# Performance work log

Measured on AMD Instinct MI355X. Metric: run time of the kernel, lower is better.

## Reference

```python
import jax, jax.numpy as jnp
import numpy as np

N_NODES = 50000
N_EDGES = 800000
DIM = 64
N_LAYERS = 5


def setup_inputs() -> dict:
    key = jax.random.key(0)
    k1, k2, k3, k4, k5 = jax.random.split(key, 5)
    x = jax.random.normal(k1, (N_NODES, DIM), dtype=jnp.float32)
    # 3 weight matrices per GIN layer (2 hidden + 1 output Dense, all [dim,dim], relu, no bias)
    W = jax.random.normal(k2, (N_LAYERS, 3, DIM, DIM), dtype=jnp.float32) * (1.0 / np.sqrt(DIM))
    # per-layer read-out Dense(1, use_bias=False)
    Wl = jax.random.normal(k3, (N_LAYERS, DIM), dtype=jnp.float32) * (1.0 / np.sqrt(DIM))
    src = jax.random.randint(k4, (N_EDGES,), 0, N_NODES, dtype=jnp.int32)
    dst = jax.random.randint(k5, (N_EDGES,), 0, N_NODES, dtype=jnp.int32)
    return {"x": x, "W": W, "Wl": Wl, "src": src, "dst": dst}


def reference(x, W, Wl, src, dst):
    n = x.shape[0]
    h = x
    pooled = []  # per-layer global mean pool  [dim]
    for i in range(N_LAYERS):
        agg = h + jax.ops.segment_sum(h[src], dst, num_segments=n)  # (1+eps)*h + sum_neighbors
        h = jax.nn.relu(agg @ W[i, 0])
        h = jax.nn.relu(h @ W[i, 1])
        h = jax.nn.relu(h @ W[i, 2])
        pooled.append(jnp.mean(h, axis=0))
    # stack per-layer Dense(1) read-outs, sum over layers, sigmoid -> shape [1]
    logits = jnp.einsum("ld,ld->l", jnp.stack(pooled), Wl)  # [5]
    return jax.nn.sigmoid(jnp.sum(logits)[None])
```

## Files before the change

kernel.cpp:

```cpp
#include <hip/hip_runtime.h>
#include <hip/hip_fp16.h>
#include <math.h>

#define N_NODES 50000
#define N_EDGES 800000
#define DIM 64
#define N_LAYERS 5

#define BLK 128
#define ROWS 32
#define HSTRIDE 68
#define POOL_REP 16

#define NB 196
#define CAPB 5632
#define EPB (N_EDGES / 256)

#define EBCAP 512

#define WFRAG_PER_LAYER (3 * 2 * 4 * 64 * 8)
#define XP (N_NODES * DIM / 4)
#define WP (N_LAYERS * WFRAG_PER_LAYER)

typedef __attribute__((ext_vector_type(8))) short short8;
typedef __attribute__((ext_vector_type(4))) float floatx4;

__device__ inline unsigned short bf16_rne(float f) {
    unsigned int u = __float_as_uint(f);
    return (unsigned short)((u + 0x7FFFu + ((u >> 16) & 1u)) >> 16);
}
__device__ inline float bf16_f(unsigned short h) {
    return __uint_as_float(((unsigned int)h) << 16);
}
__device__ inline float e5m2_f32(unsigned char b) {
    return __half2float(__ushort_as_half((unsigned short)((unsigned short)b << 8)));
}
__device__ inline unsigned char f32_e5m2(float f) {
    unsigned short us = __half_as_ushort(__float2half(f));
    us = (unsigned short)(us + 0x7F + ((us >> 8) & 1));
    return (unsigned char)(us >> 8);
}
__device__ inline __half2 e5m2x2_lo(unsigned d) {
    unsigned h = __builtin_amdgcn_perm(0u, d, 0x01050004u);
    return __builtin_bit_cast(__half2, h);
}
__device__ inline __half2 e5m2x2_hi(unsigned d) {
    unsigned h = __builtin_amdgcn_perm(0u, d, 0x03070206u);
    return __builtin_bit_cast(__half2, h);
}

__global__ __launch_bounds__(256) void prep_kernel(const float* __restrict__ x,
                                                   const float* __restrict__ W,
                                                   unsigned char* __restrict__ x8,
                                                   unsigned short* __restrict__ wfrag,
                                                   int* __restrict__ bucketCnt,
                                                   float* __restrict__ pooled) {
    int i = blockIdx.x * 256 + threadIdx.x;
    if (i < XP) {
        float4 v = ((const float4*)x)[i];
        uchar4 u;
        u.x = f32_e5m2(v.x); u.y = f32_e5m2(v.y);
        u.z = f32_e5m2(v.z); u.w = f32_e5m2(v.w);
        ((uchar4*)x8)[i] = u;
        return;
    }
    i -= XP;
    if (i < WP) {
        int t = i;
        int j    = t & 7;
        int lane = (t >> 3) & 63;
        int nt   = (t >> 9) & 3;
        int kt   = (t >> 11) & 1;
        int rest = t >> 12;
        int p    = rest % 3;
        int layer= rest / 3;
        int k = kt * 32 + (lane >> 4) * 8 + j;
        int n = nt * 16 + (lane & 15);
        float v = W[(((size_t)layer * 3 + p) * 64 + k) * 64 + n];
        wfrag[t] = bf16_rne(v);
        return;
    }
    i -= WP;
    if (i < NB) { bucketCnt[i] = 0; return; }
    i -= NB;
    if (i < N_LAYERS * POOL_REP * DIM) pooled[i] = 0.f;
}

__global__ __launch_bounds__(256) void bfill2_kernel(const int* __restrict__ src,
                                                     const int* __restrict__ dst,
                                                     int* __restrict__ bucketCnt,
                                                     int* __restrict__ ebuf) {
    __shared__ int cnt[NB];
    __shared__ int basev[NB];
    const int t = threadIdx.x;
    const int e0 = blockIdx.x * EPB;
    if (t < NB) cnt[t] = 0;
    __syncthreads();
    for (int i = t; i < EPB; i += 256)
        atomicAdd(&cnt[dst[e0 + i] >> 8], 1);
    __syncthreads();
    if (t < NB) {
        int c = cnt[t];
        basev[t] = c ? atomicAdd(&bucketCnt[t], c) : 0;
        cnt[t] = 0;
    }
    __syncthreads();
    for (int i = t; i < EPB; i += 256) {
        int d = dst[e0 + i];
        int b = d >> 8;
        int pos = atomicAdd(&cnt[b], 1);
        ebuf[(size_t)b * CAPB + basev[b] + pos] = ((d & 255) << 16) | src[e0 + i];
    }
}

__global__ __launch_bounds__(256) void bbuild_kernel(const int* __restrict__ ebuf,
                                                     const int* __restrict__ bucketCnt,
                                                     int* __restrict__ rowptr,
                                                     int* __restrict__ csr_src) {
    __shared__ int red[256];
    __shared__ int cnt[256];
    __shared__ int scan[256];
    __shared__ int cur[256];
    __shared__ int lds_e[CAPB];
    const int t = threadIdx.x;
    const int b = blockIdx.x;

    red[t] = (t < b && t < NB) ? bucketCnt[t] : 0;
    __syncthreads();
    #pragma unroll
    for (int off = 128; off > 0; off >>= 1) {
        if (t < off) red[t] += red[t + off];
        __syncthreads();
    }
    const int base  = red[0];
    const int cnt_b = bucketCnt[b];
    const int* __restrict__ ereg = ebuf + (size_t)b * CAPB;

    cnt[t] = 0;
    __syncthreads();
    for (int i = t; i < cnt_b; i += 256) {
        int v = ereg[i];
        lds_e[i] = v;
        atomicAdd(&cnt[v >> 16], 1);
    }
    __syncthreads();
    scan[t] = cnt[t];
    __syncthreads();
    #pragma unroll
    for (int off = 1; off < 256; off <<= 1) {
        int u = (t >= off) ? scan[t - off] : 0;
        __syncthreads();
        scan[t] += u;
        __syncthreads();
    }
    int excl = scan[t] - cnt[t];
    rowptr[b * 256 + t] = base + excl;
    cur[t] = excl;
    __syncthreads();
    for (int i = t; i < cnt_b; i += 256) {
        int v = lds_e[i];
        int pos = atomicAdd(&cur[v >> 16], 1);
        csr_src[base + pos] = v & 0xFFFF;
    }
}

__global__ __launch_bounds__(BLK) void layer_kernel(const unsigned char* __restrict__ h8,
                                                    const int* __restrict__ rowptr,
                                                    const int* __restrict__ csr_src,
                                                    const unsigned short* __restrict__ wf,
                                                    unsigned char* __restrict__ h_out,
                                                    float* __restrict__ pooled) {
    __shared__ float H[ROWS * HSTRIDE];
    __shared__ int EB[2][EBCAP];
    const int tid  = threadIdx.x;
    const int lane = tid & 63;
    const int w    = __builtin_amdgcn_readfirstlane(tid >> 6);
    const int n0   = blockIdx.x * ROWS;
    const int nw   = n0 + w * 16;
    const int c4   = (lane & 15) << 2;
    const int q    = lane >> 4;

    int rpv = rowptr[nw + min(lane, 16)];
    const int e0w  = __builtin_amdgcn_readlane(rpv, 0);
    const int span = __builtin_amdgcn_readlane(rpv, 16) - e0w;

    if (span <= EBCAP) {
        for (int i = lane; i < span; i += 64)
            EB[w][i] = csr_src[e0w + i];
        asm volatile("s_waitcnt lgkmcnt(0)" ::: "memory");
        const int* eb = &EB[w][0];

        for (int g = 0; g < 4; ++g) {
            const int myrow = 4 * g + q;
            const int e0q = __shfl(rpv, myrow, 64);
            const int deg = __shfl(rpv, myrow + 1, 64) - e0q;
            int Rm = deg;
            Rm = max(Rm, __shfl_xor(Rm, 16, 64));
            Rm = max(Rm, __shfl_xor(Rm, 32, 64));
            const int Rpad = (Rm + 7) & ~7;
            const int rowq = nw + myrow;
            const int ob   = e0q - e0w;

            __half2 a01 = __float2half2_rn(0.f);
            __half2 a23 = __float2half2_rn(0.f);

            for (int i = 0; i < Rpad; i += 8) {
                unsigned dv[8];
                #pragma unroll
                for (int k = 0; k < 8; ++k) {
                    int ev = eb[ob + i + k];
                    int s  = (i + k < deg) ? ev : rowq;
                    dv[k] = *(const unsigned*)(h8 + (((unsigned)s << 6) | (unsigned)c4));
                }
                #pragma unroll
                for (int k = 0; k < 8; ++k) {
                    a01 = __hadd2(a01, e5m2x2_lo(dv[k]));
                    a23 = __hadd2(a23, e5m2x2_hi(dv[k]));
                }
            }

            unsigned sd = *(const unsigned*)(h8 + (((unsigned)rowq << 6) | (unsigned)c4));
            float scale = (float)(1 - (Rpad - deg));
            float2 f01 = __half22float2(a01);
            float2 f23 = __half22float2(a23);
            float4 r;
            r.x = f01.x + e5m2_f32((unsigned char)(sd      )) * scale;
            r.y = f01.y + e5m2_f32((unsigned char)(sd >>  8)) * scale;
            r.z = f23.x + e5m2_f32((unsigned char)(sd >> 16)) * scale;
            r.w = f23.y + e5m2_f32((unsigned char)(sd >> 24)) * scale;
            if (rowq >= N_NODES) { r.x = 0.f; r.y = 0.f; r.z = 0.f; r.w = 0.f; }
            *(float4*)&H[(w * 16 + myrow) * HSTRIDE + c4] = r;
        }
    } else {
        for (int j = 0; j < 16; ++j) {
            const int n = nw + j;
            const int e0 = __builtin_amdgcn_readlane(rpv, j);
            const int e1 = __builtin_amdgcn_readlane(rpv, j + 1);
            float acc = 0.f;
            if (n < N_NODES) {
                float self = e5m2_f32(h8[(size_t)n * DIM + lane]);
                acc = self;
                for (int base = e0; base < e1; base += 64) {
                    const int m  = min(64, e1 - base);
                    const int mr = (m + 3) & ~3;
                    int idx = (lane < m) ? csr_src[base + lane] : n;
                    acc -= (float)(mr - m) * self;
                    for (int jj = 0; jj < mr; jj += 4) {
                        int s0 = __builtin_amdgcn_readlane(idx, jj + 0);
                        int s1 = __builtin_amdgcn_readlane(idx, jj + 1);
                        int s2 = __builtin_amdgcn_readlane(idx, jj + 2);
                        int s3 = __builtin_amdgcn_readlane(idx, jj + 3);
                        float v0 = e5m2_f32(h8[(size_t)s0 * DIM + lane]);
                        float v1 = e5m2_f32(h8[(size_t)s1 * DIM + lane]);
                        float v2 = e5m2_f32(h8[(size_t)s2 * DIM + lane]);
                        float v3 = e5m2_f32(h8[(size_t)s3 * DIM + lane]);
                        acc += (v0 + v1) + (v2 + v3);
                    }
                }
            }
            H[(w * 16 + j) * HSTRIDE + lane] = acc;
        }
    }
    __syncthreads();

    const int mrow = lane & 15;
    const int quad = lane >> 4;
    const short8* Bf = (const short8*)wf;

    for (int p = 0; p < 3; ++p) {
        short8 Ahi[2];
        #pragma unroll
        for (int kt = 0; kt < 2; ++kt) {
            const float* ap = &H[(w * 16 + mrow) * HSTRIDE + kt * 32 + quad * 8];
            float4 f0 = *(const float4*)ap;
            float4 f1 = *(const float4*)(ap + 4);
            float fv[8] = {f0.x, f0.y, f0.z, f0.w, f1.x, f1.y, f1.z, f1.w};
            short8 hi;
            #pragma unroll
            for (int jj = 0; jj < 8; ++jj)
                hi[jj] = (short)bf16_rne(fv[jj]);
            Ahi[kt] = hi;
        }

        floatx4 acc[4];
        #pragma unroll
        for (int nt = 0; nt < 4; ++nt) { acc[nt][0]=0.f; acc[nt][1]=0.f; acc[nt][2]=0.f; acc[nt][3]=0.f; }

        #pragma unroll
        for (int nt = 0; nt < 4; ++nt) {
            #pragma unroll
            for (int kt = 0; kt < 2; ++kt) {
                int fbase = ((p * 2 + kt) * 4 + nt) * 64 + lane;
                short8 bhi = Bf[fbase];
                acc[nt] = __builtin_amdgcn_mfma_f32_16x16x32_bf16(Ahi[kt], bhi, acc[nt], 0, 0, 0);
            }
        }
        __syncthreads();
        #pragma unroll
        for (int nt = 0; nt < 4; ++nt) {
            #pragma unroll
            for (int reg = 0; reg < 4; ++reg) {
                int row = w * 16 + quad * 4 + reg;
                H[row * HSTRIDE + nt * 16 + mrow] = fmaxf(acc[nt][reg], 0.f);
            }
        }
        __syncthreads();
    }

    #pragma unroll
    for (int i = 0; i < 4; ++i) {
        int t4 = tid + i * BLK;
        int r  = t4 >> 4;
        int c  = (t4 & 15) << 2;
        int grow = n0 + r;
        if (grow < N_NODES) {
            float4 v = *(const float4*)&H[r * HSTRIDE + c];
            uchar4 u;
            u.x = f32_e5m2(v.x); u.y = f32_e5m2(v.y);
            u.z = f32_e5m2(v.z); u.w = f32_e5m2(v.w);
            *(uchar4*)(h_out + (size_t)grow * DIM + c) = u;
        }
    }

    if (tid < 64) {
        float s = 0.f;
        #pragma unroll
        for (int r = 0; r < ROWS; ++r)
            s += H[r * HSTRIDE + tid];
        atomicAdd(&pooled[(blockIdx.x & (POOL_REP - 1)) * DIM + tid], s);
    }
}

__global__ void finalize_kernel(const float* __restrict__ pooled,
                                const float* __restrict__ Wl,
                                float* __restrict__ out) {
    int c = threadIdx.x;
    float s = 0.f;
    #pragma unroll
    for (int l = 0; l < N_LAYERS; ++l) {
        float col = 0.f;
        #pragma unroll
        for (int r = 0; r < POOL_REP; ++r)
            col += pooled[(l * POOL_REP + r) * DIM + c];
        s += col * Wl[l * DIM + c];
    }
    #pragma unroll
    for (int off = 32; off > 0; off >>= 1)
        s += __shfl_down(s, off, 64);
    if (c == 0) {
        float logit = s / (float)N_NODES;
        out[0] = 1.f / (1.f + expf(-logit));
    }
}

extern "C" void kernel_launch(void* const* d_in, const int* in_sizes, int n_in,
                              void* d_out, int out_size, void* d_ws, size_t ws_size,
                              hipStream_t stream) {
    const float* x   = (const float*)d_in[0];
    const float* W   = (const float*)d_in[1];
    const float* Wl  = (const float*)d_in[2];
    const int*   src = (const int*)d_in[3];
    const int*   dst = (const int*)d_in[4];
    float* out = (float*)d_out;

    char* ws = (char*)d_ws;
    const size_t h8Bytes = (size_t)N_NODES * DIM;
    unsigned char* hX = (unsigned char*)(ws);
    unsigned char* hA = (unsigned char*)(ws + h8Bytes);
    unsigned char* hB = (unsigned char*)(ws + 2 * h8Bytes);
    int*   csr_src  = (int*)  (ws + 3 * h8Bytes);
    int*   ebuf     = csr_src + N_EDGES;
    int*   rowptr   = ebuf + (size_t)NB * CAPB;
    int*   bucketCnt= rowptr + NB * 256;
    float* pooled   = (float*)(bucketCnt + NB);
    unsigned short* wfrag = (unsigned short*)(pooled + N_LAYERS * POOL_REP * DIM);

    const int prepItems = XP + WP + NB + N_LAYERS * POOL_REP * DIM;
    prep_kernel<<<(prepItems + 255) / 256, 256, 0, stream>>>(x, W, hX, wfrag, bucketCnt, pooled);
    bfill2_kernel<<<256, 256, 0, stream>>>(src, dst, bucketCnt, ebuf);
    bbuild_kernel<<<NB, 256, 0, stream>>>(ebuf, bucketCnt, rowptr, csr_src);

    const unsigned char* hcur = hX;
    unsigned char* hnext = hA;
    const int grid = (N_NODES + ROWS - 1) / ROWS;
    for (int l = 0; l < N_LAYERS; ++l) {
        layer_kernel<<<grid, BLK, 0, stream>>>(
            hcur, rowptr, csr_src, wfrag + (size_t)l * WFRAG_PER_LAYER, hnext,
            pooled + (size_t)l * POOL_REP * DIM);
        hcur = hnext;
        hnext = (hnext == hA) ? hB : hA;
    }
    finalize_kernel<<<1, 64, 0, stream>>>(pooled, Wl, out);
}
```

Measured before the change: 192.8 us.

## Widen gather loads, pre-shift CSR indices, drop block barriers, retune CSR build

The gather phase now has each lane load 8 bytes (uint2) covering 8 features, so each group of 8 lanes serves one row and a wave walks 16 rows in two passes instead of four. Source indices are stored pre-shifted by 6 in LDS to save address arithmetic. The per-MLP-layer __syncthreads are replaced by wave-local LDS waits, relying on each wave only touching its own 16 rows. The CSR build now uses 512 fill blocks and a 512-thread build kernel with shuffle-based reductions and scans instead of LDS tree loops. Together these aim to cut gather instruction count, barrier stalls and preprocessing latency, at some risk of LDS ordering hazards if any cross-wave sharing remains.

Result: faster. 186.4 us (-3.3%).

```diff
diff --git a/kernel.cpp b/kernel.cpp
--- a/kernel.cpp
+++ b/kernel.cpp
@@ -14,7 +14,8 @@
 
 #define NB 196
 #define CAPB 5632
-#define EPB (N_EDGES / 256)
+#define BF2_BLOCKS 512
+#define EPB2 ((N_EDGES + BF2_BLOCKS - 1) / BF2_BLOCKS)
 
 #define EBCAP 512
 
@@ -28,9 +29,6 @@
 __device__ inline unsigned short bf16_rne(float f) {
     unsigned int u = __float_as_uint(f);
     return (unsigned short)((u + 0x7FFFu + ((u >> 16) & 1u)) >> 16);
-}
-__device__ inline float bf16_f(unsigned short h) {
-    return __uint_as_float(((unsigned int)h) << 16);
 }
 __device__ inline float e5m2_f32(unsigned char b) {
     return __half2float(__ushort_as_half((unsigned short)((unsigned short)b << 8)));
@@ -93,11 +91,13 @@
     __shared__ int cnt[NB];
     __shared__ int basev[NB];
     const int t = threadIdx.x;
-    const int e0 = blockIdx.x * EPB;
+    const int e0 = blockIdx.x * EPB2;
     if (t < NB) cnt[t] = 0;
     __syncthreads();
-    for (int i = t; i < EPB; i += 256)
-        atomicAdd(&cnt[dst[e0 + i] >> 8], 1);
+    for (int i = t; i < EPB2; i += 256) {
+        int e = e0 + i;
+        if (e < N_EDGES) atomicAdd(&cnt[dst[e] >> 8], 1);
+    }
     __syncthreads();
     if (t < NB) {
         int c = cnt[t];
@@ -105,62 +105,73 @@
         cnt[t] = 0;
     }
     __syncthreads();
-    for (int i = t; i < EPB; i += 256) {
-        int d = dst[e0 + i];
-        int b = d >> 8;
-        int pos = atomicAdd(&cnt[b], 1);
-        ebuf[(size_t)b * CAPB + basev[b] + pos] = ((d & 255) << 16) | src[e0 + i];
-    }
-}
-
-__global__ __launch_bounds__(256) void bbuild_kernel(const int* __restrict__ ebuf,
+    for (int i = t; i < EPB2; i += 256) {
+        int e = e0 + i;
+        if (e < N_EDGES) {
+            int d = dst[e];
+            int b = d >> 8;
+            int pos = atomicAdd(&cnt[b], 1);
+            ebuf[(size_t)b * CAPB + basev[b] + pos] = ((d & 255) << 16) | src[e];
+        }
+    }
+}
+
+__global__ __launch_bounds__(512) void bbuild_kernel(const int* __restrict__ ebuf,
                                                      const int* __restrict__ bucketCnt,
                                                      int* __restrict__ rowptr,
                                                      int* __restrict__ csr_src) {
-    __shared__ int red[256];
     __shared__ int cnt[256];
-    __shared__ int scan[256];
     __shared__ int cur[256];
+    __shared__ int wred[8];
+    __shared__ int wscan[4];
     __shared__ int lds_e[CAPB];
     const int t = threadIdx.x;
+    const int lane = t & 63;
+    const int wv = t >> 6;
     const int b = blockIdx.x;
 
-    red[t] = (t < b && t < NB) ? bucketCnt[t] : 0;
-    __syncthreads();
+    int v = (t < b && t < NB) ? bucketCnt[t] : 0;
     #pragma unroll
-    for (int off = 128; off > 0; off >>= 1) {
-        if (t < off) red[t] += red[t + off];
-        __syncthreads();
-    }
-    const int base  = red[0];
+    for (int off = 32; off > 0; off >>= 1) v += __shfl_xor(v, off, 64);
+    if (lane == 0) wred[wv] = v;
+    if (t < 256) cnt[t] = 0;
+    __syncthreads();
+    const int base  = wred[0] + wred[1] + wred[2] + wred[3];
     const int cnt_b = bucketCnt[b];
     const int* __restrict__ ereg = ebuf + (size_t)b * CAPB;
 
-    cnt[t] = 0;
-    __syncthreads();
-    for (int i = t; i < cnt_b; i += 256) {
-        int v = ereg[i];
-        lds_e[i] = v;
-        atomicAdd(&cnt[v >> 16], 1);
-    }
-    __syncthreads();
-    scan[t] = cnt[t];
-    __syncthreads();
-    #pragma unroll
-    for (int off = 1; off < 256; off <<= 1) {
-        int u = (t >= off) ? scan[t - off] : 0;
-        __syncthreads();
-        scan[t] += u;
-        __syncthreads();
-    }
-    int excl = scan[t] - cnt[t];
-    rowptr[b * 256 + t] = base + excl;
-    cur[t] = excl;
-    __syncthreads();
-    for (int i = t; i < cnt_b; i += 256) {
-        int v = lds_e[i];
-        int pos = atomicAdd(&cur[v >> 16], 1);
-        csr_src[base + pos] = v & 0xFFFF;
+    for (int i = t; i < cnt_b; i += 512) {
+        int e = ereg[i];
+        lds_e[i] = e;
+        atomicAdd(&cnt[e >> 16], 1);
+    }
+    __syncthreads();
+
+    int excl = 0;
+    if (t < 256) {
+        int s = cnt[t];
+        #pragma unroll
+        for (int off = 1; off < 64; off <<= 1) {
+            int u = __shfl_up(s, off, 64);
+            if (lane >= off) s += u;
+        }
+        if (lane == 63) wscan[wv] = s;
+        excl = s - cnt[t];
+    }
+    __syncthreads();
+    if (t < 256) {
+        int woff = 0;
+        #pragma unroll
+        for (int j = 0; j < 4; ++j) if (j < wv) woff += wscan[j];
+        excl += woff;
+        rowptr[b * 256 + t] = base + excl;
+        cur[t] = excl;
+    }
+    __syncthreads();
+    for (int i = t; i < cnt_b; i += 512) {
+        int e = lds_e[i];
+        int pos = atomicAdd(&cur[e >> 16], 1);
+        csr_src[base + pos] = e & 0xFFFF;
     }
 }
 
@@ -177,8 +188,8 @@
     const int w    = __builtin_amdgcn_readfirstlane(tid >> 6);
     const int n0   = blockIdx.x * ROWS;
     const int nw   = n0 + w * 16;
-    const int c4   = (lane & 15) << 2;
-    const int q    = lane >> 4;
+    const int o8   = (lane & 7) << 3;
+    const int rg   = lane >> 3;
 
     int rpv = rowptr[nw + min(lane, 16)];
     const int e0w  = __builtin_amdgcn_readlane(rpv, 0);
@@ -186,50 +197,63 @@
 
     if (span <= EBCAP) {
         for (int i = lane; i < span; i += 64)
-            EB[w][i] = csr_src[e0w + i];
+            EB[w][i] = csr_src[e0w + i] << 6;
         asm volatile("s_waitcnt lgkmcnt(0)" ::: "memory");
         const int* eb = &EB[w][0];
 
-        for (int g = 0; g < 4; ++g) {
-            const int myrow = 4 * g + q;
+        for (int g = 0; g < 2; ++g) {
+            const int myrow = g * 8 + rg;
             const int e0q = __shfl(rpv, myrow, 64);
             const int deg = __shfl(rpv, myrow + 1, 64) - e0q;
             int Rm = deg;
+            Rm = max(Rm, __shfl_xor(Rm, 8, 64));
             Rm = max(Rm, __shfl_xor(Rm, 16, 64));
             Rm = max(Rm, __shfl_xor(Rm, 32, 64));
             const int Rpad = (Rm + 7) & ~7;
             const int rowq = nw + myrow;
+            const int rq6  = rowq << 6;
             const int ob   = e0q - e0w;
 
             __half2 a01 = __float2half2_rn(0.f);
-            __half2 a23 = __float2half2_rn(0.f);
+            __half2 a23 = a01, a45 = a01, a67 = a01;
 
             for (int i = 0; i < Rpad; i += 8) {
-                unsigned dv[8];
+                uint2 dv[8];
                 #pragma unroll
                 for (int k = 0; k < 8; ++k) {
-                    int ev = eb[ob + i + k];
-                    int s  = (i + k < deg) ? ev : rowq;
-                    dv[k] = *(const unsigned*)(h8 + (((unsigned)s << 6) | (unsigned)c4));
+                    int s6 = eb[ob + i + k];
+                    s6 = (i + k < deg) ? s6 : rq6;
+                    dv[k] = *(const uint2*)(h8 + (unsigned)(s6 | o8));
                 }
                 #pragma unroll
                 for (int k = 0; k < 8; ++k) {
-                    a01 = __hadd2(a01, e5m2x2_lo(dv[k]));
-                    a23 = __hadd2(a23, e5m2x2_hi(dv[k]));
+                    a01 = __hadd2(a01, e5m2x2_lo(dv[k].x));
+                    a23 = __hadd2(a23, e5m2x2_hi(dv[k].x));
+                    a45 = __hadd2(a45, e5m2x2_lo(dv[k].y));
+                    a67 = __hadd2(a67, e5m2x2_hi(dv[k].y));
                 }
             }
 
-            unsigned sd = *(const unsigned*)(h8 + (((unsigned)rowq << 6) | (unsigned)c4));
+            uint2 sd = *(const uint2*)(h8 + (unsigned)(rq6 | o8));
             float scale = (float)(1 - (Rpad - deg));
-            float2 f01 = __half22float2(a01);
-            float2 f23 = __half22float2(a23);
-            float4 r;
-            r.x = f01.x + e5m2_f32((unsigned char)(sd      )) * scale;
-            r.y = f01.y + e5m2_f32((unsigned char)(sd >>  8)) * scale;
-            r.z = f23.x + e5m2_f32((unsigned char)(sd >> 16)) * scale;
-            r.w = f23.y + e5m2_f32((unsigned char)(sd >> 24)) * scale;
-            if (rowq >= N_NODES) { r.x = 0.f; r.y = 0.f; r.z = 0.f; r.w = 0.f; }
-            *(float4*)&H[(w * 16 + myrow) * HSTRIDE + c4] = r;
+            float2 f01 = __half22float2(a01), f23 = __half22float2(a23);
+            float2 f45 = __half22float2(a45), f67 = __half22float2(a67);
+            float4 r0, r1;
+            r0.x = f01.x + e5m2_f32((unsigned char)(sd.x      )) * scale;
+            r0.y = f01.y + e5m2_f32((unsigned char)(sd.x >>  8)) * scale;
+            r0.z = f23.x + e5m2_f32((unsigned char)(sd.x >> 16)) * scale;
+            r0.w = f23.y + e5m2_f32((unsigned char)(sd.x >> 24)) * scale;
+            r1.x = f45.x + e5m2_f32((unsigned char)(sd.y      )) * scale;
+            r1.y = f45.y + e5m2_f32((unsigned char)(sd.y >>  8)) * scale;
+            r1.z = f67.x + e5m2_f32((unsigned char)(sd.y >> 16)) * scale;
+            r1.w = f67.y + e5m2_f32((unsigned char)(sd.y >> 24)) * scale;
+            if (rowq >= N_NODES) {
+                r0.x = 0.f; r0.y = 0.f; r0.z = 0.f; r0.w = 0.f;
+                r1.x = 0.f; r1.y = 0.f; r1.z = 0.f; r1.w = 0.f;
+            }
+            float* hp = &H[(w * 16 + myrow) * HSTRIDE + o8];
+            *(float4*)hp = r0;
+            *(float4*)(hp + 4) = r1;
         }
     } else {
         for (int j = 0; j < 16; ++j) {
@@ -261,7 +285,7 @@
             H[(w * 16 + j) * HSTRIDE + lane] = acc;
         }
     }
-    __syncthreads();
+    asm volatile("s_waitcnt lgkmcnt(0)" ::: "memory");
 
     const int mrow = lane & 15;
     const int quad = lane >> 4;
@@ -295,7 +319,6 @@
                 acc[nt] = __builtin_amdgcn_mfma_f32_16x16x32_bf16(Ahi[kt], bhi, acc[nt], 0, 0, 0);
             }
         }
-        __syncthreads();
         #pragma unroll
         for (int nt = 0; nt < 4; ++nt) {
             #pragma unroll
@@ -304,8 +327,8 @@
                 H[row * HSTRIDE + nt * 16 + mrow] = fmaxf(acc[nt][reg], 0.f);
             }
         }
-        __syncthreads();
-    }
+    }
+    __syncthreads();
 
     #pragma unroll
     for (int i = 0; i < 4; ++i) {
@@ -377,8 +400,8 @@
 
     const int prepItems = XP + WP + NB + N_LAYERS * POOL_REP * DIM;
     prep_kernel<<<(prepItems + 255) / 256, 256, 0, stream>>>(x, W, hX, wfrag, bucketCnt, pooled);
-    bfill2_kernel<<<256, 256, 0, stream>>>(src, dst, bucketCnt, ebuf);
-    bbuild_kernel<<<NB, 256, 0, stream>>>(ebuf, bucketCnt, rowptr, csr_src);
+    bfill2_kernel<<<BF2_BLOCKS, 256, 0, stream>>>(src, dst, bucketCnt, ebuf);
+    bbuild_kernel<<<NB, 512, 0, stream>>>(ebuf, bucketCnt, rowptr, csr_src);
 
     const unsigned char* hcur = hX;
     unsigned char* hnext = hA;
```
